# Performance work log

Measured on AMD Instinct MI355X. Metric: run time of the kernel, lower is better.

## Reference

```python
import jax, jax.numpy as jnp
import numpy as np

B, N, A, O, D, QD = 32, 64, 32, 32, 512, 512

def setup_inputs() -> dict:
    key = jax.random.key(0)
    ks = jax.random.split(key, 6)
    q = jax.random.normal(ks[0], (B, N, 1, QD), jnp.float32)
    att1 = jax.random.uniform(ks[1], (B, N, A, O), jnp.float32)
    obj_reps = jax.random.normal(ks[2], (B, O, D), jnp.float32)
    tags_attention = jax.random.randint(ks[3], (B, N, A), 0, 2).astype(jnp.int32)
    t_rep = jax.random.normal(ks[4], (B, N, A, D), jnp.float32)
    # BilinearMatrixAttention params: W [q_dim, v_dim], scalar bias
    W = jax.random.normal(ks[5], (QD, D), jnp.float32) * (1.0 / np.sqrt(QD))
    bias = jnp.zeros((), jnp.float32)
    return {"q": q, "att1": att1, "obj_reps": obj_reps,
            "tags_attention": tags_attention, "t_rep": t_rep,
            "W": W, "bias": bias, "t": 1}

def reference(q, att1, obj_reps, tags_attention, t_rep, W, bias, t):
    # v_ = einsum('bnao,bod->bnad'); v = v_ + t_rep    [b,n,a,d]
    v = jnp.einsum('bnao,bod->bnad', att1, obj_reps) + t_rep
    # bilinear attention logits: q W v^T + bias -> [b,n,a]
    qf = q[:, :, 0, :]                                  # [b,n,qd]
    inter = jnp.einsum('bnq,qd->bnd', qf, W)            # [b,n,d]
    logits = jnp.einsum('bnd,bnad->bna', inter, v) + bias
    # allennlp-style masked_softmax with temperature t
    m = tags_attention.astype(logits.dtype)             # [b,n,a]
    s = jax.nn.softmax((logits / t) * m, axis=-1) * m
    att2 = s / (jnp.sum(s, axis=-1, keepdims=True) + 1e-13)
    # attention_last = att2[:,:,None,:] @ att1 -> [b,n,o]
    return jnp.einsum('bna,bnao->bno', att2, att1)
```

## Files before the change

kernel.cpp:

```cpp
#include <hip/hip_runtime.h>


#define GM 2048
#define GK 512
#define GN 512

#define BM 32
#define BN 64
#define BK 32

__global__ __launch_bounds__(256) void gemm_qw(const float* __restrict__ A,
                                               const float* __restrict__ Bm,
                                               float* __restrict__ C) {
    __shared__ float As[BK][BM + 1];
    __shared__ float Bs[BK][BN];

    const int tid = threadIdx.x;
    const int bm0 = blockIdx.y * BM;
    const int bn0 = blockIdx.x * BN;
    const int tx = tid & 15;
    const int ty = tid >> 4;

    const int ar = tid >> 3;
    const int ak = (tid & 7) << 2;
    const int br = tid >> 4;
    const int bc = (tid & 15) << 2;

    float acc[2][4] = {};

    for (int k0 = 0; k0 < GK; k0 += BK) {
        float4 av = *(const float4*)(A + (bm0 + ar) * GK + k0 + ak);
        As[ak + 0][ar] = av.x;
        As[ak + 1][ar] = av.y;
        As[ak + 2][ar] = av.z;
        As[ak + 3][ar] = av.w;
        float4 bv0 = *(const float4*)(Bm + (k0 + br) * GN + bn0 + bc);
        float4 bv1 = *(const float4*)(Bm + (k0 + br + 16) * GN + bn0 + bc);
        *(float4*)&Bs[br][bc]      = bv0;
        *(float4*)&Bs[br + 16][bc] = bv1;
        __syncthreads();
#pragma unroll
        for (int kk = 0; kk < BK; ++kk) {
            float a0 = As[kk][ty * 2 + 0];
            float a1 = As[kk][ty * 2 + 1];
            float b0 = Bs[kk][tx * 4 + 0];
            float b1 = Bs[kk][tx * 4 + 1];
            float b2 = Bs[kk][tx * 4 + 2];
            float b3 = Bs[kk][tx * 4 + 3];
            acc[0][0] += a0 * b0; acc[0][1] += a0 * b1;
            acc[0][2] += a0 * b2; acc[0][3] += a0 * b3;
            acc[1][0] += a1 * b0; acc[1][1] += a1 * b1;
            acc[1][2] += a1 * b2; acc[1][3] += a1 * b3;
        }
        __syncthreads();
    }
#pragma unroll
    for (int i = 0; i < 2; ++i) {
        float4 v = make_float4(acc[i][0], acc[i][1], acc[i][2], acc[i][3]);
        *(float4*)(C + (bm0 + ty * 2 + i) * GN + bn0 + tx * 4) = v;
    }
}

__global__ __launch_bounds__(256) void fused_att(
    const float* __restrict__ att1, const float* __restrict__ obj_reps,
    const int* __restrict__ tags, const float* __restrict__ t_rep,
    const float* __restrict__ inter, const float* __restrict__ bias_p,
    const int* __restrict__ t_p, float* __restrict__ out) {
    const int bn = blockIdx.x;
    const int b  = bn >> 6;
    const int tid = threadIdx.x;

    __shared__ float inter_s[512];
    __shared__ float att1_s[32 * 33];
    __shared__ float proj_s[32];
    __shared__ float tdot_s[32];
    __shared__ float att2_s[32];

    {
        float2 v = *(const float2*)(inter + bn * 512 + tid * 2);
        inter_s[tid * 2 + 0] = v.x;
        inter_s[tid * 2 + 1] = v.y;
    }
    {
        float4 v = *(const float4*)(att1 + bn * 1024 + tid * 4);
        int f = tid * 4;
        int r = f >> 5, c = f & 31;
        att1_s[r * 33 + c + 0] = v.x;
        att1_s[r * 33 + c + 1] = v.y;
        att1_s[r * 33 + c + 2] = v.z;
        att1_s[r * 33 + c + 3] = v.w;
    }
    __syncthreads();

    const int g = tid >> 3;
    const int j = tid & 7;

    {
        const float* p = obj_reps + (b * 32 + g) * 512;
        float s = 0.f;
#pragma unroll
        for (int i = 0; i < 16; ++i) {
            int d = i * 32 + j * 4;
            float4 v = *(const float4*)(p + d);
            s += v.x * inter_s[d + 0] + v.y * inter_s[d + 1]
               + v.z * inter_s[d + 2] + v.w * inter_s[d + 3];
        }
        s += __shfl_xor(s, 1); s += __shfl_xor(s, 2); s += __shfl_xor(s, 4);
        if (j == 0) proj_s[g] = s;
    }
    {
        const float* p = t_rep + (bn * 32 + g) * 512;
        float s = 0.f;
#pragma unroll
        for (int i = 0; i < 16; ++i) {
            int d = i * 32 + j * 4;
            float4 v = *(const float4*)(p + d);
            s += v.x * inter_s[d + 0] + v.y * inter_s[d + 1]
               + v.z * inter_s[d + 2] + v.w * inter_s[d + 3];
        }
        s += __shfl_xor(s, 1); s += __shfl_xor(s, 2); s += __shfl_xor(s, 4);
        if (j == 0) tdot_s[g] = s;
    }
    __syncthreads();

    if (tid < 32) {
        const int a = tid;
        const float bias = *bias_p;
        const float tt = (float)(*t_p);
        float lsum = tdot_s[a] + bias;
#pragma unroll
        for (int o = 0; o < 32; ++o)
            lsum += att1_s[a * 33 + o] * proj_s[o];
        const float m = (float)tags[bn * 32 + a];
        float x = (lsum / tt) * m;
        float mx = x;
        mx = fmaxf(mx, __shfl_xor(mx, 1));
        mx = fmaxf(mx, __shfl_xor(mx, 2));
        mx = fmaxf(mx, __shfl_xor(mx, 4));
        mx = fmaxf(mx, __shfl_xor(mx, 8));
        mx = fmaxf(mx, __shfl_xor(mx, 16));
        float e = __expf(x - mx);
        float den = e;
        den += __shfl_xor(den, 1);
        den += __shfl_xor(den, 2);
        den += __shfl_xor(den, 4);
        den += __shfl_xor(den, 8);
        den += __shfl_xor(den, 16);
        float s = (e / den) * m;
        float ss = s;
        ss += __shfl_xor(ss, 1);
        ss += __shfl_xor(ss, 2);
        ss += __shfl_xor(ss, 4);
        ss += __shfl_xor(ss, 8);
        ss += __shfl_xor(ss, 16);
        att2_s[a] = s / (ss + 1e-13f);
    }
    __syncthreads();

    if (tid < 32) {
        const int o = tid;
        float s = 0.f;
#pragma unroll
        for (int a = 0; a < 32; ++a)
            s += att2_s[a] * att1_s[a * 33 + o];
        out[bn * 32 + o] = s;
    }
}

extern "C" void kernel_launch(void* const* d_in, const int* in_sizes, int n_in,
                              void* d_out, int out_size, void* d_ws, size_t ws_size,
                              hipStream_t stream) {
    const float* q        = (const float*)d_in[0];
    const float* att1     = (const float*)d_in[1];
    const float* obj_reps = (const float*)d_in[2];
    const int*   tags     = (const int*)d_in[3];
    const float* t_rep    = (const float*)d_in[4];
    const float* W        = (const float*)d_in[5];
    const float* bias_p   = (const float*)d_in[6];
    const int*   t_p      = (const int*)d_in[7];
    float* out = (float*)d_out;

    float* inter = (float*)d_ws;

    dim3 g1(GN / BN, GM / BM);
    gemm_qw<<<g1, 256, 0, stream>>>(q, W, inter);

    fused_att<<<2048, 256, 0, stream>>>(att1, obj_reps, tags, t_rep, inter,
                                        bias_p, t_p, out);
}
```

Baseline: 238.2 us.

## Enlarge q·W GEMM tile to 64x64 with 4x4 microtiles and register prefetch

The q·W GEMM now uses 64-row tiles with a 4x4 per-thread microtile read via float4 from padded shared memory. The next K-slice is prefetched into registers while the current one is computed. This is meant to cut LDS traffic per FMA and hide global load latency. It halves the block count, which may reduce occupancy and parallelism on a GPU with many compute units.

```diff
diff --git a/kernel.cpp b/kernel.cpp
--- a/kernel.cpp
+++ b/kernel.cpp
@@ -5,59 +5,75 @@
 #define GK 512
 #define GN 512
 
-#define BM 32
+#define BM 64
 #define BN 64
 #define BK 32
+#define ASTRIDE (BM + 4)
 
 __global__ __launch_bounds__(256) void gemm_qw(const float* __restrict__ A,
                                                const float* __restrict__ Bm,
                                                float* __restrict__ C) {
-    __shared__ float As[BK][BM + 1];
+    __shared__ float As[BK][ASTRIDE];
     __shared__ float Bs[BK][BN];
 
     const int tid = threadIdx.x;
     const int bm0 = blockIdx.y * BM;
     const int bn0 = blockIdx.x * BN;
-    const int tx = tid & 15;
-    const int ty = tid >> 4;
 
     const int ar = tid >> 3;
     const int ak = (tid & 7) << 2;
     const int br = tid >> 4;
     const int bc = (tid & 15) << 2;
 
-    float acc[2][4] = {};
+    const int tx = tid & 15;
+    const int ty = tid >> 4;
+
+    float acc[4][4] = {};
+
+    const float* Ab = A + (long)bm0 * GK;
+    const float* Bb = Bm + bn0;
+
+    float4 a0 = *(const float4*)(Ab + ar * GK + ak);
+    float4 a1 = *(const float4*)(Ab + (ar + 32) * GK + ak);
+    float4 b0 = *(const float4*)(Bb + br * GN + bc);
+    float4 b1 = *(const float4*)(Bb + (br + 16) * GN + bc);
 
     for (int k0 = 0; k0 < GK; k0 += BK) {
-        float4 av = *(const float4*)(A + (bm0 + ar) * GK + k0 + ak);
-        As[ak + 0][ar] = av.x;
-        As[ak + 1][ar] = av.y;
-        As[ak + 2][ar] = av.z;
-        As[ak + 3][ar] = av.w;
-        float4 bv0 = *(const float4*)(Bm + (k0 + br) * GN + bn0 + bc);
-        float4 bv1 = *(const float4*)(Bm + (k0 + br + 16) * GN + bn0 + bc);
-        *(float4*)&Bs[br][bc]      = bv0;
-        *(float4*)&Bs[br + 16][bc] = bv1;
         __syncthreads();
+        As[ak + 0][ar] = a0.x; As[ak + 1][ar] = a0.y;
+        As[ak + 2][ar] = a0.z; As[ak + 3][ar] = a0.w;
+        As[ak + 0][ar + 32] = a1.x; As[ak + 1][ar + 32] = a1.y;
+        As[ak + 2][ar + 32] = a1.z; As[ak + 3][ar + 32] = a1.w;
+        *(float4*)&Bs[br][bc]      = b0;
+        *(float4*)&Bs[br + 16][bc] = b1;
+        __syncthreads();
+
+        if (k0 + BK < GK) {
+            a0 = *(const float4*)(Ab + ar * GK + (k0 + BK) + ak);
+            a1 = *(const float4*)(Ab + (ar + 32) * GK + (k0 + BK) + ak);
+            b0 = *(const float4*)(Bb + (k0 + BK + br) * GN + bc);
+            b1 = *(const float4*)(Bb + (k0 + BK + br + 16) * GN + bc);
+        }
+
 #pragma unroll
         for (int kk = 0; kk < BK; ++kk) {
-            float a0 = As[kk][ty * 2 + 0];
-            float a1 = As[kk][ty * 2 + 1];
-            float b0 = Bs[kk][tx * 4 + 0];
-            float b1 = Bs[kk][tx * 4 + 1];
-            float b2 = Bs[kk][tx * 4 + 2];
-            float b3 = Bs[kk][tx * 4 + 3];
-            acc[0][0] += a0 * b0; acc[0][1] += a0 * b1;
-            acc[0][2] += a0 * b2; acc[0][3] += a0 * b3;
-            acc[1][0] += a1 * b0; acc[1][1] += a1 * b1;
-            acc[1][2] += a1 * b2; acc[1][3] += a1 * b3;
-        }
-        __syncthreads();
-    }
-#pragma unroll
-    for (int i = 0; i < 2; ++i) {
+            float4 av = *(const float4*)&As[kk][ty * 4];
+            float4 bv = *(const float4*)&Bs[kk][tx * 4];
+            acc[0][0] += av.x * bv.x; acc[0][1] += av.x * bv.y;
+            acc[0][2] += av.x * bv.z; acc[0][3] += av.x * bv.w;
+            acc[1][0] += av.y * bv.x; acc[1][1] += av.y * bv.y;
+            acc[1][2] += av.y * bv.z; acc[1][3] += av.y * bv.w;
+            acc[2][0] += av.z * bv.x; acc[2][1] += av.z * bv.y;
+            acc[2][2] += av.z * bv.z; acc[2][3] += av.z * bv.w;
+            acc[3][0] += av.w * bv.x; acc[3][1] += av.w * bv.y;
+            acc[3][2] += av.w * bv.z; acc[3][3] += av.w * bv.w;
+        }
+    }
+
+#pragma unroll
+    for (int i = 0; i < 4; ++i) {
         float4 v = make_float4(acc[i][0], acc[i][1], acc[i][2], acc[i][3]);
-        *(float4*)(C + (bm0 + ty * 2 + i) * GN + bn0 + tx * 4) = v;
+        *(float4*)(C + (long)(bm0 + ty * 4 + i) * GN + bn0 + tx * 4) = v;
     }
 }
 
```

Measured after the change: 233.8 us, median of 2. No clear change (-1.8%).
